# Performance work log

Hardware: AMD Instinct MI355X
Metric: run time of the kernel (lower is better)

## Reference

```python
import jax, jax.numpy as jnp
import numpy as np

B, S, D = 64, 4096, 64          # bsz*n_heads, seq_len, head_size
WINDOW = 256                    # num_toks_attended
NEG = -10000.0


def setup_inputs() -> dict:
    key = jax.random.key(0)
    kq, kk, kv = jax.random.split(key, 3)
    q = jax.random.normal(kq, (B, S, D), dtype=jnp.float32)
    k = jax.random.normal(kk, (B, S, D), dtype=jnp.float32)
    v = jax.random.normal(kv, (B, S, D), dtype=jnp.float32)
    return {"q": q, "k": k, "v": v}


def reference(q, k, v):
    # sliding_window_attn, topk_for_softmax=-1 (plain softmax)
    b, s, d = q.shape
    hw = WINDOW // 2                       # half window = 128
    n = s // hw                            # number of half-window bins
    split = lambda x: x.reshape(b, n, hw, d)
    bq, bk, bv = split(q), split(k), split(v)

    def cat_half_neighbours(x):
        # left-rolled, self, right-rolled half-bins -> [b, n, 3*hw, d]
        return jnp.concatenate(
            (jnp.roll(x, 1, axis=1), x, jnp.roll(x, -1, axis=1)), axis=-2)

    bk = cat_half_neighbours(bk)
    bv = cat_half_neighbours(bv)

    dots = jnp.einsum('bnid,bnjd->bnij', bq, bk) * (d ** -0.5)  # [b,n,hw,3hw]

    # mask: strict lower triangle on left block, none on middle,
    # upper-incl-diagonal on right block (as in the torch code)
    lmask = jnp.tril(jnp.ones((hw, hw), dtype=bool), -1)
    mask = jnp.concatenate((lmask, jnp.zeros_like(lmask), ~lmask), axis=-1)
    dots = jnp.where(mask, NEG, dots)

    p = jax.nn.softmax(dots, axis=-1)
    bo = jnp.einsum('bnij,bnjd->bnid', p, bv)
    return bo.reshape(b, s, d)
```

## Files before the change

### kernel.cpp

```cpp
#include <hip/hip_runtime.h>
#include <hip/hip_bf16.h>
#include <stdint.h>

using f32x4  = __attribute__((ext_vector_type(4))) float;
using bf16x8 = __attribute__((ext_vector_type(8))) __bf16;
using bf16x4 = __attribute__((ext_vector_type(4))) __bf16;
using bf16x2 = __attribute__((ext_vector_type(2))) __bf16;
typedef unsigned int u32;

#define SEQ 4096

__device__ __forceinline__ void mfma16(f32x4& acc, bf16x4 a, bf16x4 b) {
    asm volatile("v_mfma_f32_16x16x16_bf16 %0, %1, %2, %0"
                 : "+v"(acc) : "v"(a), "v"(b));
}

__global__ __launch_bounds__(1024, 4) void lattn_kern(
        const float* __restrict__ Q, const float* __restrict__ K,
        const float* __restrict__ V, float* __restrict__ O)
{
    __shared__ __bf16 Kl[512 * 64];
    __shared__ __bf16 Vt[64 * 520];

    const int tid  = threadIdx.x;
    const int wv   = tid >> 6;
    const int lane = tid & 63;
    const int g    = lane >> 4;
    const int c    = lane & 15;
    const u32 swc  = (u32)(c & 7);

    const int obid = blockIdx.x;
    const int bid  = (obid & 7) * 128 + (obid >> 3);
    const int b    = bid >> 4;
    const int qb   = bid & 15;
    const int t0   = qb * 256;
    const size_t baseB = (size_t)b * (SEQ * 64);

    #pragma unroll
    for (int it = 0; it < 4; ++it) {
        const int ch  = tid + it * 1024;
        const int row = ch >> 3, dg = ch & 7;
        const int grow = (t0 - 128 + row) & (SEQ - 1);
        const float* src = K + baseB + (size_t)grow * 64 + dg * 8;
        f32x4 k0 = *(const f32x4*)src, k1 = *(const f32x4*)(src + 4);
        bf16x8 hk;
        #pragma unroll
        for (int u = 0; u < 4; ++u) { hk[u] = (__bf16)k0[u]; hk[u + 4] = (__bf16)k1[u]; }
        *(bf16x8*)((char*)Kl + row * 128 + (((u32)dg ^ (u32)(row & 7)) << 4)) = hk;
    }

    #pragma unroll
    for (int it = 0; it < 2; ++it) {
        const int ch = tid + it * 1024;
        const int rp = ch >> 3, dg = ch & 7;
        const int grow = (t0 - 128 + 2 * rp) & (SEQ - 1);
        const float* src = V + baseB + (size_t)grow * 64 + dg * 8;
        f32x4 a0 = *(const f32x4*)src,        a1 = *(const f32x4*)(src + 4);
        f32x4 b0 = *(const f32x4*)(src + 64), b1 = *(const f32x4*)(src + 68);
        #pragma unroll
        for (int u = 0; u < 8; ++u) {
            const int d = dg * 8 + u;
            bf16x2 pv;
            pv[0] = (__bf16)((u < 4) ? a0[u] : a1[u - 4]);
            pv[1] = (__bf16)((u < 4) ? b0[u] : b1[u - 4]);
            *(bf16x2*)((char*)Vt + (u32)d * 1040u + (u32)rp * 4u) = pv;
        }
    }

    bf16x8 aq0, aq1;
    {
        const float* qp = Q + baseB + (size_t)(t0 + wv * 16 + c) * 64 + g * 8;
        f32x4 q0 = *(const f32x4*)qp,        q1 = *(const f32x4*)(qp + 4);
        f32x4 q2 = *(const f32x4*)(qp + 32), q3 = *(const f32x4*)(qp + 36);
        #pragma unroll
        for (int u = 0; u < 4; ++u) {
            aq0[u] = (__bf16)q0[u]; aq0[u + 4] = (__bf16)q1[u];
            aq1[u] = (__bf16)q2[u]; aq1[u + 4] = (__bf16)q3[u];
        }
    }

    __syncthreads();

    f32x4 s_[17];
    __builtin_amdgcn_s_setprio(1);
    #pragma unroll
    for (int lt = 0; lt < 17; ++lt) {
        const int row = 16 * wv + c + 16 * lt;
        const char* ka = (const char*)Kl + (u32)row * 128u;
        bf16x8 a0 = *(const bf16x8*)(ka + (((u32)g ^ swc) << 4));
        bf16x8 a1 = *(const bf16x8*)(ka + (((u32)(g + 4) ^ swc) << 4));
        f32x4 acc = {0.f, 0.f, 0.f, 0.f};
        acc = __builtin_amdgcn_mfma_f32_16x16x32_bf16(a0, aq0, acc, 0, 0, 0);
        acc = __builtin_amdgcn_mfma_f32_16x16x32_bf16(a1, aq1, acc, 0, 0, 0);
        s_[lt] = acc;
    }
    __builtin_amdgcn_s_setprio(0);

    const int k4 = 4 * g;
    float sum = 0.f;
    #pragma unroll
    for (int lt = 0; lt < 17; ++lt) {
        #pragma unroll
        for (int r = 0; r < 4; ++r) {
            float e = exp2f(s_[lt][r] * 0.18033688f);
            if (lt == 0)  e = (k4 + r <  c) ? 0.f : e;
            if (lt == 16) e = (k4 + r >= c) ? 0.f : e;
            s_[lt][r] = e; sum += e;
        }
    }
    sum += __shfl_xor(sum, 16, 64);
    sum += __shfl_xor(sum, 32, 64);
    const float inv = 1.0f / sum;

    bf16x4 pa[17];
    #pragma unroll
    for (int lt = 0; lt < 17; ++lt) {
        #pragma unroll
        for (int r = 0; r < 4; ++r) pa[lt][r] = (__bf16)(s_[lt][r] * inv);
    }

    f32x4 o[4] = {{0,0,0,0},{0,0,0,0},{0,0,0,0},{0,0,0,0}};
    const int cb = 16 * wv + 4 * g;
    __builtin_amdgcn_s_setprio(1);
    #pragma unroll
    for (int lt = 0; lt < 17; ++lt) {
        const int col = cb + 16 * lt;
        #pragma unroll
        for (int dt = 0; dt < 4; ++dt) {
            const int d = dt * 16 + c;
            const bf16x4 vbf = *(const bf16x4*)((const char*)Vt
                                + (u32)d * 1040u + (u32)col * 2u);
            mfma16(o[dt], pa[lt], vbf);
        }
    }
    __builtin_amdgcn_s_setprio(0);
    asm volatile("s_nop 7\n\ts_nop 7" ::);

    #pragma unroll
    for (int dt = 0; dt < 4; ++dt) {
        #pragma unroll
        for (int r = 0; r < 4; ++r) {
            const int row = t0 + wv * 16 + 4 * g + r;
            O[baseB + (size_t)row * 64 + dt * 16 + c] = o[dt][r];
        }
    }
}

extern "C" void kernel_launch(void* const* d_in, const int* in_sizes, int n_in,
                              void* d_out, int out_size, void* d_ws, size_t ws_size,
                              hipStream_t stream) {
    const float* q = (const float*)d_in[0];
    const float* k = (const float*)d_in[1];
    const float* v = (const float*)d_in[2];
    float* o = (float*)d_out;
    const int nB = in_sizes[0] / (SEQ * 64);
    dim3 grid(nB * 16), block(1024);
    hipLaunchKernelGGL(lattn_kern, grid, block, 0, stream, q, k, v, o);
}
```

Baseline: 79.18 us.

## Process four query tiles per block with ring-buffered K/V and prefetch

Each block now handles four consecutive 256-row query tiles instead of one. K and V sit in a 512-row circular LDS buffer, so the 256 overlapping rows are reused and only 256 new rows are loaded per step. Loads for the next tile's Q, K and V are issued before the PV MFMA loop to overlap global latency with compute. The cost is a grid four times smaller (256 blocks of 1024 threads), which lowers parallelism on a GPU with many CUs, plus extra registers for the prefetched data.

```diff
diff --git a/kernel.cpp b/kernel.cpp
--- a/kernel.cpp
+++ b/kernel.cpp
@@ -29,31 +29,32 @@
     const int c    = lane & 15;
     const u32 swc  = (u32)(c & 7);
 
-    const int obid = blockIdx.x;
-    const int bid  = (obid & 7) * 128 + (obid >> 3);
-    const int b    = bid >> 4;
-    const int qb   = bid & 15;
-    const int t0   = qb * 256;
+    const int b   = blockIdx.x >> 2;
+    const int qt  = blockIdx.x & 3;
+    const int t00 = qt * 1024;
     const size_t baseB = (size_t)b * (SEQ * 64);
+
+    int r0 = 384;
 
     #pragma unroll
     for (int it = 0; it < 4; ++it) {
-        const int ch  = tid + it * 1024;
+        const int ch = tid + it * 1024;
         const int row = ch >> 3, dg = ch & 7;
-        const int grow = (t0 - 128 + row) & (SEQ - 1);
+        const int grow = (t00 - 128 + row) & (SEQ - 1);
+        const int rr   = (384 + row) & 511;
         const float* src = K + baseB + (size_t)grow * 64 + dg * 8;
         f32x4 k0 = *(const f32x4*)src, k1 = *(const f32x4*)(src + 4);
         bf16x8 hk;
         #pragma unroll
         for (int u = 0; u < 4; ++u) { hk[u] = (__bf16)k0[u]; hk[u + 4] = (__bf16)k1[u]; }
-        *(bf16x8*)((char*)Kl + row * 128 + (((u32)dg ^ (u32)(row & 7)) << 4)) = hk;
-    }
-
+        *(bf16x8*)((char*)Kl + rr * 128 + (((u32)dg ^ (u32)(rr & 7)) << 4)) = hk;
+    }
     #pragma unroll
     for (int it = 0; it < 2; ++it) {
         const int ch = tid + it * 1024;
         const int rp = ch >> 3, dg = ch & 7;
-        const int grow = (t0 - 128 + 2 * rp) & (SEQ - 1);
+        const int grow = (t00 - 128 + 2 * rp) & (SEQ - 1);
+        const int col  = (384 + 2 * rp) & 511;
         const float* src = V + baseB + (size_t)grow * 64 + dg * 8;
         f32x4 a0 = *(const f32x4*)src,        a1 = *(const f32x4*)(src + 4);
         f32x4 b0 = *(const f32x4*)(src + 64), b1 = *(const f32x4*)(src + 68);
@@ -63,13 +64,13 @@
             bf16x2 pv;
             pv[0] = (__bf16)((u < 4) ? a0[u] : a1[u - 4]);
             pv[1] = (__bf16)((u < 4) ? b0[u] : b1[u - 4]);
-            *(bf16x2*)((char*)Vt + (u32)d * 1040u + (u32)rp * 4u) = pv;
+            *(bf16x2*)((char*)Vt + (u32)d * 1040u + (u32)col * 2u) = pv;
         }
     }
 
     bf16x8 aq0, aq1;
     {
-        const float* qp = Q + baseB + (size_t)(t0 + wv * 16 + c) * 64 + g * 8;
+        const float* qp = Q + baseB + (size_t)(t00 + wv * 16 + c) * 64 + g * 8;
         f32x4 q0 = *(const f32x4*)qp,        q1 = *(const f32x4*)(qp + 4);
         f32x4 q2 = *(const f32x4*)(qp + 32), q3 = *(const f32x4*)(qp + 36);
         #pragma unroll
@@ -79,69 +80,130 @@
         }
     }
 
-    __syncthreads();
-
-    f32x4 s_[17];
-    __builtin_amdgcn_s_setprio(1);
-    #pragma unroll
-    for (int lt = 0; lt < 17; ++lt) {
-        const int row = 16 * wv + c + 16 * lt;
-        const char* ka = (const char*)Kl + (u32)row * 128u;
-        bf16x8 a0 = *(const bf16x8*)(ka + (((u32)g ^ swc) << 4));
-        bf16x8 a1 = *(const bf16x8*)(ka + (((u32)(g + 4) ^ swc) << 4));
-        f32x4 acc = {0.f, 0.f, 0.f, 0.f};
-        acc = __builtin_amdgcn_mfma_f32_16x16x32_bf16(a0, aq0, acc, 0, 0, 0);
-        acc = __builtin_amdgcn_mfma_f32_16x16x32_bf16(a1, aq1, acc, 0, 0, 0);
-        s_[lt] = acc;
-    }
-    __builtin_amdgcn_s_setprio(0);
-
-    const int k4 = 4 * g;
-    float sum = 0.f;
-    #pragma unroll
-    for (int lt = 0; lt < 17; ++lt) {
-        #pragma unroll
-        for (int r = 0; r < 4; ++r) {
-            float e = exp2f(s_[lt][r] * 0.18033688f);
-            if (lt == 0)  e = (k4 + r <  c) ? 0.f : e;
-            if (lt == 16) e = (k4 + r >= c) ? 0.f : e;
-            s_[lt][r] = e; sum += e;
-        }
-    }
-    sum += __shfl_xor(sum, 16, 64);
-    sum += __shfl_xor(sum, 32, 64);
-    const float inv = 1.0f / sum;
-
-    bf16x4 pa[17];
-    #pragma unroll
-    for (int lt = 0; lt < 17; ++lt) {
-        #pragma unroll
-        for (int r = 0; r < 4; ++r) pa[lt][r] = (__bf16)(s_[lt][r] * inv);
-    }
-
-    f32x4 o[4] = {{0,0,0,0},{0,0,0,0},{0,0,0,0},{0,0,0,0}};
-    const int cb = 16 * wv + 4 * g;
-    __builtin_amdgcn_s_setprio(1);
-    #pragma unroll
-    for (int lt = 0; lt < 17; ++lt) {
-        const int col = cb + 16 * lt;
+    for (int i = 0; i < 4; ++i) {
+        const int t0 = t00 + i * 256;
+        __syncthreads();
+
+        f32x4 s_[17];
+        const int rb = r0 + 16 * wv + c;
+        __builtin_amdgcn_s_setprio(1);
+        #pragma unroll
+        for (int lt = 0; lt < 17; ++lt) {
+            const int row = (rb + 16 * lt) & 511;
+            const char* ka = (const char*)Kl + (u32)row * 128u;
+            bf16x8 a0 = *(const bf16x8*)(ka + (((u32)g ^ swc) << 4));
+            bf16x8 a1 = *(const bf16x8*)(ka + (((u32)(g + 4) ^ swc) << 4));
+            f32x4 acc = {0.f, 0.f, 0.f, 0.f};
+            acc = __builtin_amdgcn_mfma_f32_16x16x32_bf16(a0, aq0, acc, 0, 0, 0);
+            acc = __builtin_amdgcn_mfma_f32_16x16x32_bf16(a1, aq1, acc, 0, 0, 0);
+            s_[lt] = acc;
+        }
+        __builtin_amdgcn_s_setprio(0);
+
+        f32x4 qn0, qn1, qn2, qn3;
+        if (i < 3) {
+            const float* qp = Q + baseB + (size_t)(t0 + 256 + wv * 16 + c) * 64 + g * 8;
+            qn0 = *(const f32x4*)qp;        qn1 = *(const f32x4*)(qp + 4);
+            qn2 = *(const f32x4*)(qp + 32); qn3 = *(const f32x4*)(qp + 36);
+        }
+
+        const int k4 = 4 * g;
+        float sum = 0.f;
+        #pragma unroll
+        for (int lt = 0; lt < 17; ++lt) {
+            #pragma unroll
+            for (int r = 0; r < 4; ++r) {
+                float e = exp2f(s_[lt][r] * 0.18033688f);
+                if (lt == 0)  e = (k4 + r <  c) ? 0.f : e;
+                if (lt == 16) e = (k4 + r >= c) ? 0.f : e;
+                s_[lt][r] = e; sum += e;
+            }
+        }
+        sum += __shfl_xor(sum, 16, 64);
+        sum += __shfl_xor(sum, 32, 64);
+        const float inv = 1.0f / sum;
+
+        bf16x4 pa[17];
+        #pragma unroll
+        for (int lt = 0; lt < 17; ++lt) {
+            #pragma unroll
+            for (int r = 0; r < 4; ++r) pa[lt][r] = (__bf16)(s_[lt][r] * inv);
+        }
+
+        f32x4 dk0a, dk0b, dk1a, dk1b, dv[4];
+        int krow0 = 0, krow1 = 0, vcol = 0;
+        const int kdg = tid & 7;
+        if (i < 3) {
+            {
+                const int row = tid >> 3;
+                const int grow = (t0 + 384 + row) & (SEQ - 1);
+                const float* s0 = K + baseB + (size_t)grow * 64 + kdg * 8;
+                dk0a = *(const f32x4*)s0; dk0b = *(const f32x4*)(s0 + 4);
+                krow0 = (r0 + row) & 511;
+                const int grow1 = (t0 + 384 + row + 128) & (SEQ - 1);
+                const float* s1 = K + baseB + (size_t)grow1 * 64 + kdg * 8;
+                dk1a = *(const f32x4*)s1; dk1b = *(const f32x4*)(s1 + 4);
+                krow1 = (r0 + row + 128) & 511;
+            }
+            {
+                const int rp = tid >> 3;
+                const int grow = (t0 + 384 + 2 * rp) & (SEQ - 1);
+                const float* s0 = V + baseB + (size_t)grow * 64 + kdg * 8;
+                dv[0] = *(const f32x4*)s0;        dv[1] = *(const f32x4*)(s0 + 4);
+                dv[2] = *(const f32x4*)(s0 + 64); dv[3] = *(const f32x4*)(s0 + 68);
+                vcol = (r0 + 2 * rp) & 511;
+            }
+        }
+
+        f32x4 o[4] = {{0,0,0,0},{0,0,0,0},{0,0,0,0},{0,0,0,0}};
+        const int cb = r0 + 16 * wv + 4 * g;
+        __builtin_amdgcn_s_setprio(1);
+        #pragma unroll
+        for (int lt = 0; lt < 17; ++lt) {
+            const int col = (cb + 16 * lt) & 511;
+            #pragma unroll
+            for (int dt = 0; dt < 4; ++dt) {
+                const int d = dt * 16 + c;
+                const bf16x4 vbf = *(const bf16x4*)((const char*)Vt
+                                    + (u32)d * 1040u + (u32)col * 2u);
+                mfma16(o[dt], pa[lt], vbf);
+            }
+        }
+        __builtin_amdgcn_s_setprio(0);
+        asm volatile("s_nop 7\n\ts_nop 7" ::);
+
         #pragma unroll
         for (int dt = 0; dt < 4; ++dt) {
-            const int d = dt * 16 + c;
-            const bf16x4 vbf = *(const bf16x4*)((const char*)Vt
-                                + (u32)d * 1040u + (u32)col * 2u);
-            mfma16(o[dt], pa[lt], vbf);
-        }
-    }
-    __builtin_amdgcn_s_setprio(0);
-    asm volatile("s_nop 7\n\ts_nop 7" ::);
-
-    #pragma unroll
-    for (int dt = 0; dt < 4; ++dt) {
-        #pragma unroll
-        for (int r = 0; r < 4; ++r) {
-            const int row = t0 + wv * 16 + 4 * g + r;
-            O[baseB + (size_t)row * 64 + dt * 16 + c] = o[dt][r];
+            #pragma unroll
+            for (int r = 0; r < 4; ++r) {
+                const int row = t0 + wv * 16 + 4 * g + r;
+                O[baseB + (size_t)row * 64 + dt * 16 + c] = o[dt][r];
+            }
+        }
+
+        if (i < 3) {
+            __syncthreads();
+            bf16x8 hk;
+            #pragma unroll
+            for (int u = 0; u < 4; ++u) { hk[u] = (__bf16)dk0a[u]; hk[u + 4] = (__bf16)dk0b[u]; }
+            *(bf16x8*)((char*)Kl + krow0 * 128 + (((u32)kdg ^ (u32)(krow0 & 7)) << 4)) = hk;
+            #pragma unroll
+            for (int u = 0; u < 4; ++u) { hk[u] = (__bf16)dk1a[u]; hk[u + 4] = (__bf16)dk1b[u]; }
+            *(bf16x8*)((char*)Kl + krow1 * 128 + (((u32)kdg ^ (u32)(krow1 & 7)) << 4)) = hk;
+            #pragma unroll
+            for (int u = 0; u < 8; ++u) {
+                const int d = kdg * 8 + u;
+                bf16x2 pv;
+                pv[0] = (__bf16)((u < 4) ? dv[0][u] : dv[1][u - 4]);
+                pv[1] = (__bf16)((u < 4) ? dv[2][u] : dv[3][u - 4]);
+                *(bf16x2*)((char*)Vt + (u32)d * 1040u + (u32)vcol * 2u) = pv;
+            }
+            r0 = (r0 + 256) & 511;
+            #pragma unroll
+            for (int u = 0; u < 4; ++u) {
+                aq0[u] = (__bf16)qn0[u]; aq0[u + 4] = (__bf16)qn1[u];
+                aq1[u] = (__bf16)qn2[u]; aq1[u + 4] = (__bf16)qn3[u];
+            }
         }
     }
 }
@@ -154,6 +216,6 @@
     const float* v = (const float*)d_in[2];
     float* o = (float*)d_out;
     const int nB = in_sizes[0] / (SEQ * 64);
-    dim3 grid(nB * 16), block(1024);
+    dim3 grid(nB * 4), block(1024);
     hipLaunchKernelGGL(lattn_kern, grid, block, 0, stream, q, k, v, o);
 }
```

Result: slower. 116.3 us (+46.9%).
